# Kernel tuning notes

Measured on AMD Instinct MI355X. Metric: run time of the kernel, lower is better.

The kernel has to match this reference:

```python
import jax, jax.numpy as jnp
import numpy as np

OUT = 56          # roi_align / mask resolution
SCALE = 0.25      # spatial_scale (bases at stride 4)
CO = 14           # raw coefficient resolution


def _roi_align_one(feat, box):
    """torchvision roi_align, aligned=True, sampling_ratio=1.
    feat: [B, H, W] base maps for this roi's image; box: [4] = (x0,y0,x1,y1).
    Returns [B, OUT, OUT]."""
    H, W = feat.shape[1], feat.shape[2]
    s = box * SCALE - 0.5  # aligned=True half-pixel offset
    x0, y0, x1, y1 = s[0], s[1], s[2], s[3]
    bw = (x1 - x0) / OUT
    bh = (y1 - y0) / OUT
    # sampling_ratio=1 -> single sample at each bin center
    xs = x0 + (jnp.arange(OUT, dtype=feat.dtype) + 0.5) * bw
    ys = y0 + (jnp.arange(OUT, dtype=feat.dtype) + 0.5) * bh
    vy = (ys >= -1.0) & (ys <= H)
    vx = (xs >= -1.0) & (xs <= W)
    yc = jnp.clip(ys, 0.0, H - 1)
    xc = jnp.clip(xs, 0.0, W - 1)
    yl = jnp.clip(jnp.floor(yc).astype(jnp.int32), 0, H - 2); yh = yl + 1
    xl = jnp.clip(jnp.floor(xc).astype(jnp.int32), 0, W - 2); xh = xl + 1
    ly = yc - yl; hy = 1.0 - ly
    lx = xc - xl; hx = 1.0 - lx
    fll = feat[:, yl, :][:, :, xl]; flh = feat[:, yl, :][:, :, xh]
    fhl = feat[:, yh, :][:, :, xl]; fhh = feat[:, yh, :][:, :, xh]
    val = (hy[:, None] * (hx[None, :] * fll + lx[None, :] * flh)
           + ly[:, None] * (hx[None, :] * fhl + lx[None, :] * fhh))
    return val * (vy[:, None] & vx[None, :])


def _paste_masks(masks, boxes, img_h, img_w):
    """do_paste_mask: grid_sample(bilinear, align_corners=False, zero pad).
    The grid is separable (y depends on row, x on column), so express it as two
    batched matmuls with tent-kernel weights. masks: [N,56,56] -> [N,img_h,img_w]."""
    x0, y0, x1, y1 = (boxes[:, 0:1], boxes[:, 1:2], boxes[:, 2:3], boxes[:, 3:4])
    gy = ((jnp.arange(img_h, dtype=masks.dtype) + 0.5 - y0) / (y1 - y0)) * 2.0 - 1.0  # [N,H]
    gx = ((jnp.arange(img_w, dtype=masks.dtype) + 0.5 - x0) / (x1 - x0)) * 2.0 - 1.0  # [N,W]
    # unnormalize (align_corners=False): f = (g+1)*size/2 - 0.5
    fy = (gy + 1.0) * OUT * 0.5 - 0.5
    fx = (gx + 1.0) * OUT * 0.5 - 0.5
    idx = jnp.arange(OUT, dtype=masks.dtype)
    Wy = jnp.maximum(0.0, 1.0 - jnp.abs(fy[:, :, None] - idx))  # [N, img_h, 56]
    Wx = jnp.maximum(0.0, 1.0 - jnp.abs(fx[:, :, None] - idx))  # [N, img_w, 56]
    rows = jnp.einsum('nhm,nmw->nhw', Wy, masks)                # [N, img_h, 56]
    return jnp.einsum('nhw,nqw->nhq', rows, Wx)                 # [N, img_h, img_w]


def setup_inputs() -> dict:
    key = jax.random.key(0)
    ks = jax.random.split(key, 6)
    b_h, b_w = 136, 200                 # bases at stride 4 of a 544x800 image
    img_h, img_w = b_h * 4, b_w * 4
    N, Bb = 100, 4
    bases = jax.random.normal(ks[0], (1, Bb, b_h, b_w), jnp.float32)
    x0 = jax.random.uniform(ks[1], (N, 1), minval=0.0, maxval=img_w * 0.55)
    y0 = jax.random.uniform(ks[2], (N, 1), minval=0.0, maxval=img_h * 0.55)
    w = jax.random.uniform(ks[3], (N, 1), minval=32.0, maxval=img_w * 0.4)
    h = jax.random.uniform(ks[4], (N, 1), minval=32.0, maxval=img_h * 0.4)
    boxes = jnp.concatenate([x0, y0,
                             jnp.minimum(x0 + w, img_w - 1.0),
                             jnp.minimum(y0 + h, img_h - 1.0)], axis=1)
    top = jax.random.normal(ks[5], (N, Bb * CO * CO), jnp.float32)
    box_feat = jnp.concatenate([jnp.zeros((N, 1), jnp.float32), boxes, top], axis=1)
    return {"bases": bases, "box_feat": box_feat}


def reference(bases, box_feat):
    bidx = box_feat[:, 0].astype(jnp.int32)
    boxes = box_feat[:, 1:5]
    top_feat = box_feat[:, 5:]
    N = box_feat.shape[0]
    Bb, b_h, b_w = bases.shape[1], bases.shape[2], bases.shape[3]
    # roi_align over all detections
    rois = jax.vmap(lambda i, b: _roi_align_one(bases[i], b))(bidx, boxes)  # [N,B,56,56]
    # merge_bases: upsample 14->56 (bilinear, align_corners=False), softmax over bases, blend
    coeffs = top_feat.reshape(N, Bb, CO, CO)
    coeffs = jax.image.resize(coeffs, (N, Bb, OUT, OUT), method='bilinear')
    coeffs = jax.nn.softmax(coeffs, axis=1)
    masks = jax.nn.sigmoid(jnp.sum(rois * coeffs, axis=1))  # [N,56,56]
    return _paste_masks(masks, boxes, b_h * 4, b_w * 4)      # [N, 4*b_h, 4*b_w]
```

## Files before the change

kernel.cpp:

```cpp
#include <hip/hip_runtime.h>
#include <math.h>

#define OUTD 56
#define COD  14
#define BH   136
#define BW   200
#define IMGH 544
#define IMGW 800
#define BB   4
#define BFS  789
#define GRP  8
#define W4   (IMGW / 4)
#define ELEMS (GRP * W4)

__global__ __launch_bounds__(256) void mask_kernel(
    const float* __restrict__ bases,
    const float* __restrict__ box_feat,
    float* __restrict__ masks) {
  const int n = blockIdx.y;
  const int p = blockIdx.x * 256 + threadIdx.x;
  if (p >= OUTD * OUTD) return;
  const int y = p / OUTD;
  const int x = p - y * OUTD;

  const float* bf = box_feat + (size_t)n * BFS;
  const int bidx = (int)bf[0];
  const float x0 = bf[1], y0 = bf[2], x1 = bf[3], y1 = bf[4];
  const float sx0 = x0 * 0.25f - 0.5f;
  const float sy0 = y0 * 0.25f - 0.5f;
  const float bwv = (x1 - x0) * 0.25f * (1.0f / OUTD);
  const float bhv = (y1 - y0) * 0.25f * (1.0f / OUTD);
  const float* feat = bases + (size_t)bidx * BB * BH * BW;
  const float* top  = bf + 5;

  const float ysv = sy0 + ((float)y + 0.5f) * bhv;
  const float xsv = sx0 + ((float)x + 0.5f) * bwv;
  const float valid =
      (ysv >= -1.0f && ysv <= (float)BH && xsv >= -1.0f && xsv <= (float)BW)
          ? 1.0f : 0.0f;
  const float yc = fminf(fmaxf(ysv, 0.0f), (float)(BH - 1));
  const float xc = fminf(fmaxf(xsv, 0.0f), (float)(BW - 1));
  int yl = (int)floorf(yc); yl = yl > (BH - 2) ? (BH - 2) : yl;
  int xl = (int)floorf(xc); xl = xl > (BW - 2) ? (BW - 2) : xl;
  const float ly = yc - (float)yl, hy = 1.0f - ly;
  const float lx = xc - (float)xl, hx = 1.0f - lx;
  const float w00 = hy * hx, w01 = hy * lx, w10 = ly * hx, w11 = ly * lx;

  float cyf = fminf(fmaxf(((float)y + 0.5f) * 0.25f - 0.5f, 0.0f), (float)(COD - 1));
  float cxf = fminf(fmaxf(((float)x + 0.5f) * 0.25f - 0.5f, 0.0f), (float)(COD - 1));
  int cyl = (int)floorf(cyf); cyl = cyl > (COD - 2) ? (COD - 2) : cyl;
  int cxl = (int)floorf(cxf); cxl = cxl > (COD - 2) ? (COD - 2) : cxl;
  const float cly = cyf - (float)cyl, chy = 1.0f - cly;
  const float clx = cxf - (float)cxl, chx = 1.0f - clx;
  const float cw00 = chy * chx, cw01 = chy * clx, cw10 = cly * chx, cw11 = cly * clx;

  float rvals[BB], cvals[BB];
#pragma unroll
  for (int b = 0; b < BB; ++b) {
    const float* fb = feat + b * BH * BW;
    const float r = w00 * fb[yl * BW + xl]       + w01 * fb[yl * BW + xl + 1] +
                    w10 * fb[(yl + 1) * BW + xl] + w11 * fb[(yl + 1) * BW + xl + 1];
    rvals[b] = r * valid;
    const float* tb = top + b * COD * COD;
    cvals[b] = cw00 * tb[cyl * COD + cxl]       + cw01 * tb[cyl * COD + cxl + 1] +
               cw10 * tb[(cyl + 1) * COD + cxl] + cw11 * tb[(cyl + 1) * COD + cxl + 1];
  }

  const float mx = fmaxf(fmaxf(cvals[0], cvals[1]), fmaxf(cvals[2], cvals[3]));
  float e[BB], s = 0.0f;
#pragma unroll
  for (int b = 0; b < BB; ++b) { e[b] = __expf(cvals[b] - mx); s += e[b]; }
  const float inv = 1.0f / s;
  float dot = 0.0f;
#pragma unroll
  for (int b = 0; b < BB; ++b) dot += rvals[b] * (e[b] * inv);
  masks[(size_t)n * (OUTD * OUTD) + p] = 1.0f / (1.0f + __expf(-dot));
}

__global__ __launch_bounds__(256) void paste_group(
    const float* __restrict__ masks,
    const float* __restrict__ box_feat,
    float4* __restrict__ out) {
  const int n  = blockIdx.y;
  const int hs = (int)blockIdx.x * GRP;
  const int tid = threadIdx.x;

  const float* bf = box_feat + (size_t)n * BFS;
  const float x0 = bf[1], y0 = bf[2], x1 = bf[3], y1 = bf[4];

  float4* obase = out + ((size_t)n * IMGH + hs) * W4;

  const float sy = (float)OUTD / (y1 - y0);
  const float cyc_ = (0.5f - y0) * sy - 0.5f;
  const float fy_first = (float)hs * sy + cyc_;
  const float fy_last  = (float)(hs + GRP - 1) * sy + cyc_;

  if (!(fy_last > -1.0f && fy_first < (float)OUTD)) {
    const float4 z = make_float4(0.f, 0.f, 0.f, 0.f);
    for (int idx = tid; idx < ELEMS; idx += 256) obase[idx] = z;
    return;
  }

  __shared__ float m[OUTD * OUTD];
  {
    const float* msrc = masks + (size_t)n * (OUTD * OUTD);
    for (int i = tid; i < OUTD * OUTD; i += 256) m[i] = msrc[i];
  }
  __syncthreads();

  const float invw = (float)OUTD / (x1 - x0);
  const float cxc = (0.5f - x0) * invw - 0.5f;

  int row = tid / W4;
  int col = tid - row * W4;
  for (int idx = tid; idx < ELEMS; idx += 256) {
    const float fy = (float)(hs + row) * sy + cyc_;
    float4 o = make_float4(0.f, 0.f, 0.f, 0.f);
    if (fy > -1.0f && fy < (float)OUTD) {
      const int ml = (int)floorf(fy);
      float wy1 = fy - (float)ml;
      float wy0 = 1.0f - wy1;
      const int r0 = ml < 0 ? 0 : ml;
      const int r1 = (ml + 1 > OUTD - 1) ? (OUTD - 1) : (ml + 1);
      if (ml < 0) wy0 = 0.0f;
      if (ml + 1 > OUTD - 1) wy1 = 0.0f;
      const float* row0 = &m[r0 * OUTD];
      const float* row1 = &m[r1 * OUTD];
      float res[4];
#pragma unroll
      for (int i = 0; i < 4; ++i) {
        const float q = (float)(col * 4 + i);
        const float fx = fmaf(q, invw, cxc);
        float v = 0.0f;
        if (fx > -1.0f && fx < (float)OUTD) {
          const int xl = (int)floorf(fx);
          float wx1 = fx - (float)xl;
          float wx0 = 1.0f - wx1;
          const int xls = xl < 0 ? 0 : xl;
          const int xhs = (xl + 1 > OUTD - 1) ? (OUTD - 1) : (xl + 1);
          if (xl < 0) wx0 = 0.0f;
          if (xl + 1 > OUTD - 1) wx1 = 0.0f;
          v = wy0 * (wx0 * row0[xls] + wx1 * row0[xhs]) +
              wy1 * (wx0 * row1[xls] + wx1 * row1[xhs]);
        }
        res[i] = v;
      }
      o = make_float4(res[0], res[1], res[2], res[3]);
    }
    obase[row * W4 + col] = o;
    row += 1;
    col += 56;
    if (col >= W4) { col -= W4; row += 1; }
  }
}

extern "C" void kernel_launch(void* const* d_in, const int* in_sizes, int n_in,
                              void* d_out, int out_size, void* d_ws, size_t ws_size,
                              hipStream_t stream) {
  const float* bases    = (const float*)d_in[0];
  const float* box_feat = (const float*)d_in[1];
  const int N = in_sizes[1] / BFS;

  float* masks = (float*)d_ws;

  dim3 g1((OUTD * OUTD + 255) / 256, N);
  mask_kernel<<<g1, 256, 0, stream>>>(bases, box_feat, masks);

  dim3 g2(IMGH / GRP, N);
  paste_group<<<g2, 256, 0, stream>>>(masks, box_feat, (float4*)d_out);
}
```

Measured before the change: 180.0 us.

## Fuse mask computation into paste kernel, computing only needed mask rows per block

Removes the separate mask_kernel and its workspace round trip. Each paste block now computes, straight into shared memory, only the mask rows its output row group needs (lo..hi), running the roi_align, coefficient upsample, softmax and sigmoid math inline. This saves one kernel launch and the global write and read of the masks, but some mask rows are recomputed across neighbouring row groups, and the bases gathers now happen inside the paste blocks.

```diff
diff --git a/kernel.cpp b/kernel.cpp
--- a/kernel.cpp
+++ b/kernel.cpp
@@ -13,26 +13,9 @@
 #define W4   (IMGW / 4)
 #define ELEMS (GRP * W4)
 
-__global__ __launch_bounds__(256) void mask_kernel(
-    const float* __restrict__ bases,
-    const float* __restrict__ box_feat,
-    float* __restrict__ masks) {
-  const int n = blockIdx.y;
-  const int p = blockIdx.x * 256 + threadIdx.x;
-  if (p >= OUTD * OUTD) return;
-  const int y = p / OUTD;
-  const int x = p - y * OUTD;
-
-  const float* bf = box_feat + (size_t)n * BFS;
-  const int bidx = (int)bf[0];
-  const float x0 = bf[1], y0 = bf[2], x1 = bf[3], y1 = bf[4];
-  const float sx0 = x0 * 0.25f - 0.5f;
-  const float sy0 = y0 * 0.25f - 0.5f;
-  const float bwv = (x1 - x0) * 0.25f * (1.0f / OUTD);
-  const float bhv = (y1 - y0) * 0.25f * (1.0f / OUTD);
-  const float* feat = bases + (size_t)bidx * BB * BH * BW;
-  const float* top  = bf + 5;
-
+__device__ __forceinline__ float mask_value(
+    const float* __restrict__ feat, const float* __restrict__ top,
+    float sx0, float sy0, float bwv, float bhv, int y, int x) {
   const float ysv = sy0 + ((float)y + 0.5f) * bhv;
   const float xsv = sx0 + ((float)x + 0.5f) * bwv;
   const float valid =
@@ -74,11 +57,11 @@
   float dot = 0.0f;
 #pragma unroll
   for (int b = 0; b < BB; ++b) dot += rvals[b] * (e[b] * inv);
-  masks[(size_t)n * (OUTD * OUTD) + p] = 1.0f / (1.0f + __expf(-dot));
+  return 1.0f / (1.0f + __expf(-dot));
 }
 
-__global__ __launch_bounds__(256) void paste_group(
-    const float* __restrict__ masks,
+__global__ __launch_bounds__(256) void fused_paste(
+    const float* __restrict__ bases,
     const float* __restrict__ box_feat,
     float4* __restrict__ out) {
   const int n  = blockIdx.y;
@@ -103,8 +86,23 @@
 
   __shared__ float m[OUTD * OUTD];
   {
-    const float* msrc = masks + (size_t)n * (OUTD * OUTD);
-    for (int i = tid; i < OUTD * OUTD; i += 256) m[i] = msrc[i];
+    const int lo = max(0, (int)floorf(fy_first));
+    const int hi = min(OUTD - 1, (int)floorf(fy_last) + 1);
+    const int cnt = (hi - lo + 1) * OUTD;
+
+    const int bidx = (int)bf[0];
+    const float sx0 = x0 * 0.25f - 0.5f;
+    const float sy0 = y0 * 0.25f - 0.5f;
+    const float bwv = (x1 - x0) * 0.25f * (1.0f / OUTD);
+    const float bhv = (y1 - y0) * 0.25f * (1.0f / OUTD);
+    const float* feat = bases + (size_t)bidx * BB * BH * BW;
+    const float* top  = bf + 5;
+
+    for (int i = tid; i < cnt; i += 256) {
+      const int r = lo + i / OUTD;
+      const int x = i - (i / OUTD) * OUTD;
+      m[r * OUTD + x] = mask_value(feat, top, sx0, sy0, bwv, bhv, r, x);
+    }
   }
   __syncthreads();
 
@@ -161,11 +159,6 @@
   const float* box_feat = (const float*)d_in[1];
   const int N = in_sizes[1] / BFS;
 
-  float* masks = (float*)d_ws;
-
-  dim3 g1((OUTD * OUTD + 255) / 256, N);
-  mask_kernel<<<g1, 256, 0, stream>>>(bases, box_feat, masks);
-
-  dim3 g2(IMGH / GRP, N);
-  paste_group<<<g2, 256, 0, stream>>>(masks, box_feat, (float4*)d_out);
+  dim3 grid(IMGH / GRP, N);
+  fused_paste<<<grid, 256, 0, stream>>>(bases, box_feat, (float4*)d_out);
 }
```

Result: faster. 175.0 us (-2.8%).
